# Performance work log

Hardware: AMD Instinct MI355X
Metric: run time of the kernel (lower is better)

## Reference

```python
import jax, jax.numpy as jnp
import numpy as np

SEQ_LEN, BATCH, VOCAB, EMB, HID, NLAYERS = 64, 128, 10000, 1024, 1024, 2


def setup_inputs() -> dict:
    key = jax.random.key(0)
    ks = jax.random.split(key, 12)
    u = lambda k, shape: jax.random.uniform(k, shape, jnp.float32, -0.1, 0.1)
    inputs = jax.random.randint(ks[0], (SEQ_LEN, BATCH), 0, VOCAB)
    hidden = jnp.zeros((NLAYERS, BATCH, HID), jnp.float32)
    emb_table = u(ks[1], (VOCAB, EMB))
    # gate weights: in_features = EMB(+)HID == 2*HID since EMB==HID; stacked over layers
    Wr = u(ks[2], (NLAYERS, 2 * HID, HID)); br = jnp.zeros((NLAYERS, HID), jnp.float32)
    Wz = u(ks[3], (NLAYERS, 2 * HID, HID)); bz = jnp.zeros((NLAYERS, HID), jnp.float32)
    Wg = u(ks[4], (NLAYERS, 2 * HID, HID)); bg = jnp.zeros((NLAYERS, HID), jnp.float32)
    Wout = u(ks[5], (HID, VOCAB)); bout = jnp.zeros((VOCAB,), jnp.float32)
    return {"inputs": inputs, "hidden": hidden, "emb_table": emb_table,
            "Wr": Wr, "br": br, "Wz": Wz, "bz": bz, "Wg": Wg, "bg": bg,
            "Wout": Wout, "bout": bout}


def reference(inputs, hidden, emb_table, Wr, br, Wz, bz, Wg, bg, Wout, bout):
    # inputs: [T, B] int ids; hidden: [L, B, H]
    x = emb_table[inputs]  # [T, B, E]
    L = Wr.shape[0]

    def step(h, x_t):
        inp = x_t
        new_h = []
        for l in range(L):
            cat = jnp.concatenate([inp, h[l]], axis=-1)            # [B, 2H]
            r = jnp.tanh(cat @ Wr[l] + br[l])                      # tanh gate (as in source)
            z = jnp.tanh(cat @ Wz[l] + bz[l])
            cat2 = jnp.concatenate([inp, r * h[l]], axis=-1)
            h_tild = jnp.tanh(cat2 @ Wg[l] + bg[l])
            hn = (1.0 - z) * h[l] + z * h_tild
            inp = hn
            new_h.append(hn)
        logits_t = jnp.tanh(inp @ Wout + bout)                     # Tanh on logits (as in source)
        return jnp.stack(new_h), logits_t

    h_final, logits = jax.lax.scan(step, hidden, x)
    return logits, h_final
```

## Files before the change

### kernel.cpp

```cpp
#include <hip/hip_runtime.h>

#define T_STEPS 64
#define BATCH   128
#define HID     1024
#define VOCAB   10000
#define VPAD    10240
#define NSPLIT  8
#define KCHUNK  256

typedef unsigned short ushort_t;
typedef __attribute__((ext_vector_type(8))) short bf16x8_t;
typedef __attribute__((ext_vector_type(4))) float f32x4_t;

typedef const unsigned int __attribute__((address_space(1)))* gptr1_t;
typedef unsigned int __attribute__((address_space(3)))* lptr3_t;

#if defined(__has_builtin)
#if __has_builtin(__builtin_amdgcn_global_load_lds)
#define HAVE_GLL 1
#endif
#endif

__device__ inline unsigned short f2bf(float f) {
    unsigned int u = __float_as_uint(f);
    u += 0x7fffu + ((u >> 16) & 1u);
    return (unsigned short)(u >> 16);
}

__global__ void init_h(const float* __restrict__ hidden,
                       float* __restrict__ h0, float* __restrict__ h1)
{
    int i = blockIdx.x * blockDim.x + threadIdx.x;
    if (i < BATCH * HID) {
        h0[i] = hidden[i];
        h1[i] = hidden[BATCH * HID + i];
    }
}

__global__ void final_h(const float* __restrict__ h0, const float* __restrict__ h1,
                        float* __restrict__ out)
{
    int i = blockIdx.x * blockDim.x + threadIdx.x;
    if (i < BATCH * HID) {
        out[i] = h0[i];
        out[BATCH * HID + i] = h1[i];
    }
}

__global__ __launch_bounds__(256)
void gather_kernel(const int* __restrict__ ids, const float* __restrict__ emb,
                   float* __restrict__ xemb)
{
    const int row = blockIdx.x;
    const int c4 = threadIdx.x * 4;
    float4 v = *(const float4*)&emb[(size_t)ids[row] * HID + c4];
    *(float4*)&xemb[(size_t)row * HID + c4] = v;
}

__global__ __launch_bounds__(256)
void woutT_kernel(const float* __restrict__ Wout, ushort_t* __restrict__ WT)
{
    __shared__ float ld[32][33];
    const int v0 = blockIdx.x * 32, k0 = blockIdx.y * 32;
    const int r = threadIdx.x >> 3;
    const int c4 = (threadIdx.x & 7) * 4;
    #pragma unroll
    for (int q = 0; q < 4; ++q) {
        int v = v0 + c4 + q;
        float val = 0.0f;
        if (v < VOCAB) val = Wout[(size_t)(k0 + r) * VOCAB + v];
        ld[c4 + q][r] = val;
    }
    __syncthreads();
    ushort4 o;
    o.x = f2bf(ld[r][c4 + 0]);
    o.y = f2bf(ld[r][c4 + 1]);
    o.z = f2bf(ld[r][c4 + 2]);
    o.w = f2bf(ld[r][c4 + 3]);
    *(ushort4*)&WT[(size_t)(v0 + r) * HID + k0 + c4] = o;
}

__global__ __launch_bounds__(256)
void agemm_k(const float* __restrict__ xemb_t0,
             const float* __restrict__ h0, const float* __restrict__ h1,
             const float* __restrict__ Wr, const float* __restrict__ Wz,
             float* __restrict__ part_rz, int do0, int do1)
{
    const int layer = blockIdx.z;
    if (layer == 0 && !do0) return;
    if (layer == 1 && !do1) return;

    __shared__ float As[128 * 64];
    __shared__ float Bs[64 * 64];
    const int tid = threadIdx.x;
    const int w = tid >> 6;
    const int lane = tid & 63;
    const int lrow = lane >> 4;
    const int lchunk = lane & 15;
    const int tx = tid & 15;
    const int ty = tid >> 4;
    const int j0 = blockIdx.x * 64;
    const int kbase = blockIdx.y * KCHUNK;

    const float* W = ((j0 < HID) ? Wr : Wz) + (size_t)layer * (2 * HID * HID);
    const int jc = j0 & (HID - 1);
    const float* A_lo = layer ? h0 : xemb_t0;
    const float* A_hi = layer ? h1 : h0;

    float acc[8][4] = {};

    for (int kt0 = 0; kt0 < KCHUNK; kt0 += 64) {
        const int kg0 = kbase + kt0;
        const float* src = (kg0 < HID) ? A_lo : A_hi;
        const int kmod = kg0 & (HID - 1);
        if (kt0 > 0) __syncthreads();
        #pragma unroll
        for (int ii = 0; ii < 8; ++ii) {
            int issue = w * 8 + ii;
            int r = issue * 4 + lrow;
            int gc = (lchunk ^ (r & 3)) * 4;
            const float* ga = src + (size_t)r * HID + kmod + gc;
#ifdef HAVE_GLL
            __builtin_amdgcn_global_load_lds((gptr1_t)(const void*)ga,
                (lptr3_t)(void*)(As + issue * 256), 16, 0, 0);
#else
            *(float4*)&As[issue * 256 + lane * 4] = *(const float4*)ga;
#endif
        }
        #pragma unroll
        for (int ii = 0; ii < 4; ++ii) {
            int issue = w * 4 + ii;
            int kr = issue * 4 + lrow;
            const float* gb = W + (size_t)(kg0 + kr) * HID + jc + lchunk * 4;
#ifdef HAVE_GLL
            __builtin_amdgcn_global_load_lds((gptr1_t)(const void*)gb,
                (lptr3_t)(void*)(Bs + issue * 256), 16, 0, 0);
#else
            *(float4*)&Bs[issue * 256 + lane * 4] = *(const float4*)gb;
#endif
        }
        __syncthreads();
        #pragma unroll
        for (int kk = 0; kk < 64; kk += 4) {
            f32x4_t b[4];
            #pragma unroll
            for (int q = 0; q < 4; ++q)
                b[q] = *(const f32x4_t*)&Bs[(kk + q) * 64 + tx * 4];
            #pragma unroll
            for (int i = 0; i < 8; ++i) {
                int row = ty + i * 16;
                int cswz = (((kk >> 2) ^ (row & 3)) << 2);
                f32x4_t a = *(const f32x4_t*)&As[row * 64 + cswz];
                #pragma unroll
                for (int q = 0; q < 4; ++q) {
                    acc[i][0] += a[q] * b[q][0];
                    acc[i][1] += a[q] * b[q][1];
                    acc[i][2] += a[q] * b[q][2];
                    acc[i][3] += a[q] * b[q][3];
                }
            }
        }
    }

    float* dst = part_rz + (size_t)(layer * NSPLIT + blockIdx.y) * (BATCH * 2 * HID);
    #pragma unroll
    for (int i = 0; i < 8; ++i) {
        int row = ty + i * 16;
        float4 v;
        v.x = acc[i][0]; v.y = acc[i][1]; v.z = acc[i][2]; v.w = acc[i][3];
        *(float4*)&dst[(size_t)row * 2048 + j0 + tx * 4] = v;
    }
}

__global__ __launch_bounds__(256)
void aact_kernel(const float* __restrict__ part_rz,
                 const float* __restrict__ br,
                 const float* __restrict__ h0, const float* __restrict__ h1,
                 float* __restrict__ rh0, float* __restrict__ rh1,
                 int do0, int do1)
{
    const int layer = blockIdx.y;
    if (layer == 0 && !do0) return;
    if (layer == 1 && !do1) return;
    const int idx4 = (blockIdx.x * 256 + threadIdx.x) * 4;
    const int b = idx4 >> 10, j = idx4 & (HID - 1);
    const float* p = part_rz + (size_t)layer * NSPLIT * (BATCH * 2 * HID)
                   + (size_t)b * 2048 + j;
    float4 s = {0.f, 0.f, 0.f, 0.f};
    #pragma unroll
    for (int sp = 0; sp < NSPLIT; ++sp) {
        float4 v = *(const float4*)&p[(size_t)sp * (BATCH * 2 * HID)];
        s.x += v.x; s.y += v.y; s.z += v.z; s.w += v.w;
    }
    float4 bb = *(const float4*)&br[layer * HID + j];
    float4 hv = *(const float4*)&(layer ? h1 : h0)[idx4];
    float4 rh;
    rh.x = tanhf(s.x + bb.x) * hv.x;
    rh.y = tanhf(s.y + bb.y) * hv.y;
    rh.z = tanhf(s.z + bb.z) * hv.z;
    rh.w = tanhf(s.w + bb.w) * hv.w;
    *(float4*)&(layer ? rh1 : rh0)[idx4] = rh;
}

__global__ __launch_bounds__(256)
void bgemm_k(const float* __restrict__ xemb_t0,
             const float* __restrict__ h0, const float* __restrict__ h1,
             const float* __restrict__ rh0, const float* __restrict__ rh1,
             const float* __restrict__ Wg,
             float* __restrict__ part_g, int do0, int do1)
{
    const int layer = blockIdx.z;
    if (layer == 0 && !do0) return;
    if (layer == 1 && !do1) return;

    __shared__ float As[128 * 64];
    __shared__ float Bs[64 * 32];
    const int tid = threadIdx.x;
    const int w = tid >> 6;
    const int lane = tid & 63;
    const int lrow = lane >> 4;
    const int lchunk = lane & 15;
    const int tx = tid & 7;
    const int ty = tid >> 3;
    const int j0 = blockIdx.x * 32;
    const int kbase = blockIdx.y * KCHUNK;

    const float* W = Wg + (size_t)layer * (2 * HID * HID);
    const float* A_lo = layer ? h0 : xemb_t0;
    const float* A_hi = layer ? rh1 : rh0;

    float acc[4][4] = {};

    for (int kt0 = 0; kt0 < KCHUNK; kt0 += 64) {
        const int kg0 = kbase + kt0;
        const float* src = (kg0 < HID) ? A_lo : A_hi;
        const int kmod = kg0 & (HID - 1);
        if (kt0 > 0) __syncthreads();
        #pragma unroll
        for (int ii = 0; ii < 8; ++ii) {
            int issue = w * 8 + ii;
            int r = issue * 4 + lrow;
            int gc = (lchunk ^ (r & 3)) * 4;
            const float* ga = src + (size_t)r * HID + kmod + gc;
#ifdef HAVE_GLL
            __builtin_amdgcn_global_load_lds((gptr1_t)(const void*)ga,
                (lptr3_t)(void*)(As + issue * 256), 16, 0, 0);
#else
            *(float4*)&As[issue * 256 + lane * 4] = *(const float4*)ga;
#endif
        }
        #pragma unroll
        for (int ii = 0; ii < 2; ++ii) {
            int issue = w * 2 + ii;
            int kr = issue * 8 + (lane >> 3);
            const float* gb = W + (size_t)(kg0 + kr) * HID + j0 + (lane & 7) * 4;
#ifdef HAVE_GLL
            __builtin_amdgcn_global_load_lds((gptr1_t)(const void*)gb,
                (lptr3_t)(void*)(Bs + issue * 256), 16, 0, 0);
#else
            *(float4*)&Bs[issue * 256 + lane * 4] = *(const float4*)gb;
#endif
        }
        __syncthreads();
        #pragma unroll
        for (int kk = 0; kk < 64; kk += 4) {
            f32x4_t b[4];
            #pragma unroll
            for (int q = 0; q < 4; ++q)
                b[q] = *(const f32x4_t*)&Bs[(kk + q) * 32 + tx * 4];
            #pragma unroll
            for (int i = 0; i < 4; ++i) {
                int row = ty + i * 32;
                int cswz = (((kk >> 2) ^ (row & 3)) << 2);
                f32x4_t a = *(const f32x4_t*)&As[row * 64 + cswz];
                #pragma unroll
                for (int q = 0; q < 4; ++q) {
                    acc[i][0] += a[q] * b[q][0];
                    acc[i][1] += a[q] * b[q][1];
                    acc[i][2] += a[q] * b[q][2];
                    acc[i][3] += a[q] * b[q][3];
                }
            }
        }
    }

    float* dst = part_g + (size_t)(layer * NSPLIT + blockIdx.y) * (BATCH * HID);
    #pragma unroll
    for (int i = 0; i < 4; ++i) {
        int row = ty + i * 32;
        float4 v;
        v.x = acc[i][0]; v.y = acc[i][1]; v.z = acc[i][2]; v.w = acc[i][3];
        *(float4*)&dst[(size_t)row * HID + j0 + tx * 4] = v;
    }
}

__global__ __launch_bounds__(256)
void bact_kernel(const float* __restrict__ part_rz, const float* __restrict__ part_g,
                 const float* __restrict__ bz, const float* __restrict__ bg,
                 float* __restrict__ h0, float* __restrict__ h1,
                 ushort_t* __restrict__ h1bf, int t1, int do0, int do1)
{
    const int layer = blockIdx.y;
    if (layer == 0 && !do0) return;
    if (layer == 1 && !do1) return;
    const int idx4 = (blockIdx.x * 256 + threadIdx.x) * 4;
    const int b = idx4 >> 10, j = idx4 & (HID - 1);

    const float* pz = part_rz + (size_t)layer * NSPLIT * (BATCH * 2 * HID)
                    + (size_t)b * 2048 + HID + j;
    float4 sz = {0.f, 0.f, 0.f, 0.f};
    #pragma unroll
    for (int sp = 0; sp < NSPLIT; ++sp) {
        float4 v = *(const float4*)&pz[(size_t)sp * (BATCH * 2 * HID)];
        sz.x += v.x; sz.y += v.y; sz.z += v.z; sz.w += v.w;
    }
    float4 bzv = *(const float4*)&bz[layer * HID + j];
    float4 z;
    z.x = tanhf(sz.x + bzv.x); z.y = tanhf(sz.y + bzv.y);
    z.z = tanhf(sz.z + bzv.z); z.w = tanhf(sz.w + bzv.w);

    const float* pg = part_g + (size_t)layer * NSPLIT * (BATCH * HID) + idx4;
    float4 sg = {0.f, 0.f, 0.f, 0.f};
    #pragma unroll
    for (int sp = 0; sp < NSPLIT; ++sp) {
        float4 v = *(const float4*)&pg[(size_t)sp * (BATCH * HID)];
        sg.x += v.x; sg.y += v.y; sg.z += v.z; sg.w += v.w;
    }
    float4 bgv = *(const float4*)&bg[layer * HID + j];
    float4 g;
    g.x = tanhf(sg.x + bgv.x); g.y = tanhf(sg.y + bgv.y);
    g.z = tanhf(sg.z + bgv.z); g.w = tanhf(sg.w + bgv.w);

    float* h = layer ? h1 : h0;
    float4 hv = *(const float4*)&h[idx4];
    float4 hn;
    hn.x = (1.0f - z.x) * hv.x + z.x * g.x;
    hn.y = (1.0f - z.y) * hv.y + z.y * g.y;
    hn.z = (1.0f - z.z) * hv.z + z.z * g.z;
    hn.w = (1.0f - z.w) * hv.w + z.w * g.w;
    *(float4*)&h[idx4] = hn;

    if (layer == 1) {
        ushort4 o;
        o.x = f2bf(hn.x); o.y = f2bf(hn.y); o.z = f2bf(hn.z); o.w = f2bf(hn.w);
        *(ushort4*)&h1bf[(size_t)t1 * (BATCH * HID) + idx4] = o;
    }
}

__global__ __launch_bounds__(256)
void logits_mfma_kernel(const ushort_t* __restrict__ Abf,
                        const ushort_t* __restrict__ BT,
                        const float* __restrict__ bout,
                        float* __restrict__ out)
{
    __shared__ ushort_t As[128 * 64];
    __shared__ ushort_t Bs[128 * 64];
    const int tid = threadIdx.x;
    const int wave = tid >> 6, lane = tid & 63;
    const int m0 = blockIdx.y * 128, n0 = blockIdx.x * 128;
    const int wr = wave >> 1, wc = wave & 1;

    const int srow = lane >> 3;
    const int sch = (lane & 7) ^ (srow & 7);
    const int lrow = lane & 15, lhi = lane >> 4;

    f32x4_t acc[4][4] = {};

    for (int k0 = 0; k0 < HID; k0 += 64) {
        #pragma unroll
        for (int i = 0; i < 4; ++i) {
            int issue = wave * 4 + i;
            int row = issue * 8 + srow;
            const ushort_t* ga = Abf + (size_t)(m0 + row) * HID + k0 + sch * 8;
            const ushort_t* gb = BT + (size_t)(n0 + row) * HID + k0 + sch * 8;
#ifdef HAVE_GLL
            __builtin_amdgcn_global_load_lds((gptr1_t)(const void*)ga,
                                             (lptr3_t)(void*)(As + issue * 512), 16, 0, 0);
            __builtin_amdgcn_global_load_lds((gptr1_t)(const void*)gb,
                                             (lptr3_t)(void*)(Bs + issue * 512), 16, 0, 0);
#else
            *(bf16x8_t*)(As + issue * 512 + lane * 8) = *(const bf16x8_t*)ga;
            *(bf16x8_t*)(Bs + issue * 512 + lane * 8) = *(const bf16x8_t*)gb;
#endif
        }
        __syncthreads();

        bf16x8_t af[4][2], bfm[4][2];
        const char* Ab = (const char*)As;
        const char* Bb = (const char*)Bs;
        #pragma unroll
        for (int m = 0; m < 4; ++m) {
            int row = wr * 64 + m * 16 + lrow;
            #pragma unroll
            for (int ks = 0; ks < 2; ++ks) {
                int off = row * 128 + (((ks * 4 + lhi) ^ (lrow & 7)) * 16);
                af[m][ks] = *(const bf16x8_t*)(Ab + off);
            }
        }
        #pragma unroll
        for (int n = 0; n < 4; ++n) {
            int row = wc * 64 + n * 16 + lrow;
            #pragma unroll
            for (int ks = 0; ks < 2; ++ks) {
                int off = row * 128 + (((ks * 4 + lhi) ^ (lrow & 7)) * 16);
                bfm[n][ks] = *(const bf16x8_t*)(Bb + off);
            }
        }
        #pragma unroll
        for (int m = 0; m < 4; ++m)
            #pragma unroll
            for (int n = 0; n < 4; ++n)
                #pragma unroll
                for (int ks = 0; ks < 2; ++ks)
                    acc[m][n] = __builtin_amdgcn_mfma_f32_16x16x32_bf16(
                        af[m][ks], bfm[n][ks], acc[m][n], 0, 0, 0);
        __syncthreads();
    }

    #pragma unroll
    for (int m = 0; m < 4; ++m) {
        int row = m0 + wr * 64 + m * 16 + lhi * 4;
        #pragma unroll
        for (int n = 0; n < 4; ++n) {
            int col = n0 + wc * 64 + n * 16 + lrow;
            if (col < VOCAB) {
                float bo = bout[col];
                #pragma unroll
                for (int q = 0; q < 4; ++q)
                    out[(size_t)(row + q) * VOCAB + col] = tanhf(acc[m][n][q] + bo);
            }
        }
    }
}

extern "C" void kernel_launch(void* const* d_in, const int* in_sizes, int n_in,
                              void* d_out, int out_size, void* d_ws, size_t ws_size,
                              hipStream_t stream)
{
    const int*   inputs = (const int*)  d_in[0];
    const float* hidden = (const float*)d_in[1];
    const float* emb    = (const float*)d_in[2];
    const float* Wr     = (const float*)d_in[3];
    const float* br     = (const float*)d_in[4];
    const float* Wz     = (const float*)d_in[5];
    const float* bz     = (const float*)d_in[6];
    const float* Wg     = (const float*)d_in[7];
    const float* bg     = (const float*)d_in[8];
    const float* Wout   = (const float*)d_in[9];
    const float* bout   = (const float*)d_in[10];
    float* out = (float*)d_out;

    const size_t BH = BATCH * HID;

    float* ws = (float*)d_ws;
    float* h0      = ws;
    float* h1      = h0 + BH;
    float* rh0     = h1 + BH;
    float* rh1     = rh0 + BH;
    float* part_rz = rh1 + BH;
    float* part_g  = part_rz + 2 * NSPLIT * (BATCH * 2 * HID);
    float* xemb    = part_g + 2 * NSPLIT * (BATCH * HID);
    ushort_t* h1bf = (ushort_t*)(xemb + (size_t)T_STEPS * BH);
    ushort_t* WT   = h1bf + (size_t)T_STEPS * BH;

    init_h<<<(int)(BH + 255) / 256, 256, 0, stream>>>(hidden, h0, h1);
    gather_kernel<<<T_STEPS * BATCH, 256, 0, stream>>>(inputs, emb, xemb);
    woutT_kernel<<<dim3(VPAD / 32, HID / 32), 256, 0, stream>>>(Wout, WT);

    for (int s = 0; s <= T_STEPS; ++s) {
        int do0 = (s < T_STEPS) ? 1 : 0;
        int do1 = (s >= 1) ? 1 : 0;
        const float* xemb_t0 = xemb + (size_t)s * BH;
        agemm_k<<<dim3(32, NSPLIT, 2), 256, 0, stream>>>(
            xemb_t0, h0, h1, Wr, Wz, part_rz, do0, do1);
        aact_kernel<<<dim3(128, 2), 256, 0, stream>>>(
            part_rz, br, h0, h1, rh0, rh1, do0, do1);
        bgemm_k<<<dim3(32, NSPLIT, 2), 256, 0, stream>>>(
            xemb_t0, h0, h1, rh0, rh1, Wg, part_g, do0, do1);
        bact_kernel<<<dim3(128, 2), 256, 0, stream>>>(
            part_rz, part_g, bz, bg, h0, h1, h1bf, s - 1, do0, do1);
    }

    final_h<<<(int)(BH + 255) / 256, 256, 0, stream>>>(
        h0, h1, out + (size_t)T_STEPS * BATCH * VOCAB);

    logits_mfma_kernel<<<dim3(VPAD / 128, 8192 / 128), 256, 0, stream>>>(
        h1bf, WT, bout, out);
}
```

Measured before the change: 4.067 ms.

## Double-buffer LDS tiles in the GRU gate GEMMs to overlap loads with FMA

The r/z and candidate-gate split-K GEMM kernels switch from single-buffered 64-wide K tiles to double-buffered 32-wide K tiles. The next tile is fetched into LDS with global_load_lds while the current tile is being computed, so global load latency is meant to overlap with FMA work instead of stalling at each barrier. In exchange there are more barriers per K chunk (8 instead of 4) and smaller tiles. The LDS footprint stays the same.

```diff
diff --git a/kernel.cpp b/kernel.cpp
--- a/kernel.cpp
+++ b/kernel.cpp
@@ -90,13 +90,11 @@
     if (layer == 0 && !do0) return;
     if (layer == 1 && !do1) return;
 
-    __shared__ float As[128 * 64];
-    __shared__ float Bs[64 * 64];
+    __shared__ float As[2][128 * 32];
+    __shared__ float Bs[2][32 * 64];
     const int tid = threadIdx.x;
     const int w = tid >> 6;
     const int lane = tid & 63;
-    const int lrow = lane >> 4;
-    const int lchunk = lane & 15;
     const int tx = tid & 15;
     const int ty = tid >> 4;
     const int j0 = blockIdx.x * 64;
@@ -107,50 +105,85 @@
     const float* A_lo = layer ? h0 : xemb_t0;
     const float* A_hi = layer ? h1 : h0;
 
+    const int a_r8 = lane >> 3;
+    const int a_c  = lane & 7;
+    const int b_r4 = lane >> 4;
+    const int b_c  = lane & 15;
+
     float acc[8][4] = {};
 
-    for (int kt0 = 0; kt0 < KCHUNK; kt0 += 64) {
-        const int kg0 = kbase + kt0;
-        const float* src = (kg0 < HID) ? A_lo : A_hi;
-        const int kmod = kg0 & (HID - 1);
-        if (kt0 > 0) __syncthreads();
-        #pragma unroll
-        for (int ii = 0; ii < 8; ++ii) {
-            int issue = w * 8 + ii;
-            int r = issue * 4 + lrow;
-            int gc = (lchunk ^ (r & 3)) * 4;
-            const float* ga = src + (size_t)r * HID + kmod + gc;
+#define A_STAGE(buf, t)                                                         \
+    {                                                                           \
+        const int kg0 = kbase + (t) * 32;                                       \
+        const float* src = (kg0 < HID) ? A_lo : A_hi;                           \
+        const int kmod = kg0 & (HID - 1);                                       \
+        _Pragma("unroll")                                                       \
+        for (int ii = 0; ii < 4; ++ii) {                                        \
+            int issue = w * 4 + ii;                                  \
+            int r = issue * 8 + a_r8;                               \
+            int gc = (a_c ^ (r & 3)) * 4;                                       \
+            const float* ga = src + (size_t)r * HID + kmod + gc;                \
+            __builtin_amdgcn_global_load_lds((gptr1_t)(const void*)ga,          \
+                (lptr3_t)(void*)(&As[buf][issue * 256]), 16, 0, 0);             \
+        }                                                                       \
+        _Pragma("unroll")                                                       \
+        for (int ii = 0; ii < 2; ++ii) {                                        \
+            int issue = w * 2 + ii;                                   \
+            int kr = issue * 4 + b_r4;                               \
+            const float* gb = W + (size_t)(kg0 + kr) * HID + jc + b_c * 4;      \
+            __builtin_amdgcn_global_load_lds((gptr1_t)(const void*)gb,          \
+                (lptr3_t)(void*)(&Bs[buf][issue * 256]), 16, 0, 0);             \
+        }                                                                       \
+    }
+#define A_STAGE_F(buf, t)                                                       \
+    {                                                                           \
+        const int kg0 = kbase + (t) * 32;                                       \
+        const float* src = (kg0 < HID) ? A_lo : A_hi;                           \
+        const int kmod = kg0 & (HID - 1);                                       \
+        _Pragma("unroll")                                                       \
+        for (int ii = 0; ii < 4; ++ii) {                                        \
+            int issue = w * 4 + ii;                                             \
+            int r = issue * 8 + a_r8;                                           \
+            int gc = (a_c ^ (r & 3)) * 4;                                       \
+            *(float4*)&As[buf][issue * 256 + lane * 4] =                        \
+                *(const float4*)(src + (size_t)r * HID + kmod + gc);            \
+        }                                                                       \
+        _Pragma("unroll")                                                       \
+        for (int ii = 0; ii < 2; ++ii) {                                        \
+            int issue = w * 2 + ii;                                             \
+            int kr = issue * 4 + b_r4;                                          \
+            *(float4*)&Bs[buf][issue * 256 + lane * 4] =                        \
+                *(const float4*)(W + (size_t)(kg0 + kr) * HID + jc + b_c * 4);  \
+        }                                                                       \
+    }
+
 #ifdef HAVE_GLL
-            __builtin_amdgcn_global_load_lds((gptr1_t)(const void*)ga,
-                (lptr3_t)(void*)(As + issue * 256), 16, 0, 0);
+    A_STAGE(0, 0)
 #else
-            *(float4*)&As[issue * 256 + lane * 4] = *(const float4*)ga;
-#endif
-        }
-        #pragma unroll
-        for (int ii = 0; ii < 4; ++ii) {
-            int issue = w * 4 + ii;
-            int kr = issue * 4 + lrow;
-            const float* gb = W + (size_t)(kg0 + kr) * HID + jc + lchunk * 4;
+    A_STAGE_F(0, 0)
+#endif
+    __syncthreads();
+    #pragma unroll
+    for (int t = 0; t < 8; ++t) {
+        const int buf = t & 1;
+        if (t + 1 < 8) {
 #ifdef HAVE_GLL
-            __builtin_amdgcn_global_load_lds((gptr1_t)(const void*)gb,
-                (lptr3_t)(void*)(Bs + issue * 256), 16, 0, 0);
+            A_STAGE(buf ^ 1, t + 1)
 #else
-            *(float4*)&Bs[issue * 256 + lane * 4] = *(const float4*)gb;
-#endif
-        }
-        __syncthreads();
-        #pragma unroll
-        for (int kk = 0; kk < 64; kk += 4) {
+            A_STAGE_F(buf ^ 1, t + 1)
+#endif
+        }
+        #pragma unroll
+        for (int kk = 0; kk < 32; kk += 4) {
             f32x4_t b[4];
             #pragma unroll
             for (int q = 0; q < 4; ++q)
-                b[q] = *(const f32x4_t*)&Bs[(kk + q) * 64 + tx * 4];
+                b[q] = *(const f32x4_t*)&Bs[buf][(kk + q) * 64 + tx * 4];
             #pragma unroll
             for (int i = 0; i < 8; ++i) {
                 int row = ty + i * 16;
                 int cswz = (((kk >> 2) ^ (row & 3)) << 2);
-                f32x4_t a = *(const f32x4_t*)&As[row * 64 + cswz];
+                f32x4_t a = *(const f32x4_t*)&As[buf][row * 32 + cswz];
                 #pragma unroll
                 for (int q = 0; q < 4; ++q) {
                     acc[i][0] += a[q] * b[q][0];
@@ -160,7 +193,10 @@
                 }
             }
         }
-    }
+        __syncthreads();
+    }
+#undef A_STAGE
+#undef A_STAGE_F
 
     float* dst = part_rz + (size_t)(layer * NSPLIT + blockIdx.y) * (BATCH * 2 * HID);
     #pragma unroll
@@ -213,13 +249,11 @@
     if (layer == 0 && !do0) return;
     if (layer == 1 && !do1) return;
 
-    __shared__ float As[128 * 64];
-    __shared__ float Bs[64 * 32];
+    __shared__ float As[2][128 * 32];
+    __shared__ float Bs[2][32 * 32];
     const int tid = threadIdx.x;
     const int w = tid >> 6;
     const int lane = tid & 63;
-    const int lrow = lane >> 4;
-    const int lchunk = lane & 15;
     const int tx = tid & 7;
     const int ty = tid >> 3;
     const int j0 = blockIdx.x * 32;
@@ -229,50 +263,79 @@
     const float* A_lo = layer ? h0 : xemb_t0;
     const float* A_hi = layer ? rh1 : rh0;
 
+    const int a_r8 = lane >> 3;
+    const int a_c  = lane & 7;
+
     float acc[4][4] = {};
 
-    for (int kt0 = 0; kt0 < KCHUNK; kt0 += 64) {
-        const int kg0 = kbase + kt0;
-        const float* src = (kg0 < HID) ? A_lo : A_hi;
-        const int kmod = kg0 & (HID - 1);
-        if (kt0 > 0) __syncthreads();
-        #pragma unroll
-        for (int ii = 0; ii < 8; ++ii) {
-            int issue = w * 8 + ii;
-            int r = issue * 4 + lrow;
-            int gc = (lchunk ^ (r & 3)) * 4;
-            const float* ga = src + (size_t)r * HID + kmod + gc;
+#define B_STAGE(buf, t)                                                         \
+    {                                                                           \
+        const int kg0 = kbase + (t) * 32;                                       \
+        const float* src = (kg0 < HID) ? A_lo : A_hi;                           \
+        const int kmod = kg0 & (HID - 1);                                       \
+        _Pragma("unroll")                                                       \
+        for (int ii = 0; ii < 4; ++ii) {                                        \
+            int issue = w * 4 + ii;                                             \
+            int r = issue * 8 + a_r8;                                           \
+            int gc = (a_c ^ (r & 3)) * 4;                                       \
+            const float* ga = src + (size_t)r * HID + kmod + gc;                \
+            __builtin_amdgcn_global_load_lds((gptr1_t)(const void*)ga,          \
+                (lptr3_t)(void*)(&As[buf][issue * 256]), 16, 0, 0);             \
+        }                                                                       \
+        {                                                                       \
+            int r = w * 8 + a_r8;                                    \
+            const float* gb = W + (size_t)(kg0 + r) * HID + j0 + a_c * 4;       \
+            __builtin_amdgcn_global_load_lds((gptr1_t)(const void*)gb,          \
+                (lptr3_t)(void*)(&Bs[buf][w * 256]), 16, 0, 0);                 \
+        }                                                                       \
+    }
+#define B_STAGE_F(buf, t)                                                       \
+    {                                                                           \
+        const int kg0 = kbase + (t) * 32;                                       \
+        const float* src = (kg0 < HID) ? A_lo : A_hi;                           \
+        const int kmod = kg0 & (HID - 1);                                       \
+        _Pragma("unroll")                                                       \
+        for (int ii = 0; ii < 4; ++ii) {                                        \
+            int issue = w * 4 + ii;                                             \
+            int r = issue * 8 + a_r8;                                           \
+            int gc = (a_c ^ (r & 3)) * 4;                                       \
+            *(float4*)&As[buf][issue * 256 + lane * 4] =                        \
+                *(const float4*)(src + (size_t)r * HID + kmod + gc);            \
+        }                                                                       \
+        {                                                                       \
+            int r = w * 8 + a_r8;                                               \
+            *(float4*)&Bs[buf][w * 256 + lane * 4] =                            \
+                *(const float4*)(W + (size_t)(kg0 + r) * HID + j0 + a_c * 4);   \
+        }                                                                       \
+    }
+
 #ifdef HAVE_GLL
-            __builtin_amdgcn_global_load_lds((gptr1_t)(const void*)ga,
-                (lptr3_t)(void*)(As + issue * 256), 16, 0, 0);
+    B_STAGE(0, 0)
 #else
-            *(float4*)&As[issue * 256 + lane * 4] = *(const float4*)ga;
-#endif
-        }
-        #pragma unroll
-        for (int ii = 0; ii < 2; ++ii) {
-            int issue = w * 2 + ii;
-            int kr = issue * 8 + (lane >> 3);
-            const float* gb = W + (size_t)(kg0 + kr) * HID + j0 + (lane & 7) * 4;
+    B_STAGE_F(0, 0)
+#endif
+    __syncthreads();
+    #pragma unroll
+    for (int t = 0; t < 8; ++t) {
+        const int buf = t & 1;
+        if (t + 1 < 8) {
 #ifdef HAVE_GLL
-            __builtin_amdgcn_global_load_lds((gptr1_t)(const void*)gb,
-                (lptr3_t)(void*)(Bs + issue * 256), 16, 0, 0);
+            B_STAGE(buf ^ 1, t + 1)
 #else
-            *(float4*)&Bs[issue * 256 + lane * 4] = *(const float4*)gb;
-#endif
-        }
-        __syncthreads();
-        #pragma unroll
-        for (int kk = 0; kk < 64; kk += 4) {
+            B_STAGE_F(buf ^ 1, t + 1)
+#endif
+        }
+        #pragma unroll
+        for (int kk = 0; kk < 32; kk += 4) {
             f32x4_t b[4];
             #pragma unroll
             for (int q = 0; q < 4; ++q)
-                b[q] = *(const f32x4_t*)&Bs[(kk + q) * 32 + tx * 4];
+                b[q] = *(const f32x4_t*)&Bs[buf][(kk + q) * 32 + tx * 4];
             #pragma unroll
             for (int i = 0; i < 4; ++i) {
                 int row = ty + i * 32;
                 int cswz = (((kk >> 2) ^ (row & 3)) << 2);
-                f32x4_t a = *(const f32x4_t*)&As[row * 64 + cswz];
+                f32x4_t a = *(const f32x4_t*)&As[buf][row * 32 + cswz];
                 #pragma unroll
                 for (int q = 0; q < 4; ++q) {
                     acc[i][0] += a[q] * b[q][0];
@@ -282,7 +345,10 @@
                 }
             }
         }
-    }
+        __syncthreads();
+    }
+#undef B_STAGE
+#undef B_STAGE_F
 
     float* dst = part_g + (size_t)(layer * NSPLIT + blockIdx.y) * (BATCH * HID);
     #pragma unroll
```

Result: slower. 6.252 ms (+53.7%).
